# Performance work log

Hardware: AMD Instinct MI355X
Metric: run time of the kernel (lower is better)

## Reference

```python
import jax, jax.numpy as jnp
import numpy as np

B, T, H = 32, 2048, 1024

def setup_inputs() -> dict:
    key = jax.random.key(0)
    ks = jax.random.split(key, 9)
    s = 1.0 / np.sqrt(H)
    return {
        "encoder_outputs": jax.random.normal(ks[0], (B, T, H), jnp.float32),
        "decoder_output": jax.random.normal(ks[1], (1, B, H), jnp.float32),
        "Wk": jax.random.uniform(ks[2], (H, H), jnp.float32, -s, s),
        "bk": jax.random.uniform(ks[3], (H,), jnp.float32, -s, s),
        "Wq": jax.random.uniform(ks[4], (H, H), jnp.float32, -s, s),
        "bq": jax.random.uniform(ks[5], (H,), jnp.float32, -s, s),
        "Wout": jax.random.uniform(ks[6], (H,), jnp.float32, -s, s),
        "bout": jax.random.uniform(ks[7], (), jnp.float32, -s, s),
        "inputs": jax.random.randint(ks[8], (B, T), 0, 32000, jnp.int32),  # unused, as in original
    }

def reference(encoder_outputs, decoder_output, Wk, bk, Wq, bq, Wout, bout, inputs):
    # decoder_output: [1, B, H] -> [B, 1, H]
    dec = jnp.swapaxes(decoder_output, 0, 1)
    k = encoder_outputs @ Wk.T + bk          # [B, T, H]
    q = dec @ Wq.T + bq                      # [B, 1, H]
    score = jnp.tanh(k + q) @ Wout + bout    # [B, T]  (linear_out squeezed)
    attn = jax.nn.softmax(score, axis=-1)    # [B, T]
    context = jnp.einsum('bt,bth->bh', attn, encoder_outputs)  # [B, H]
    return context[:, None, :]               # [B, 1, H]
```

## Files before the change

kernel.cpp:

```cpp
#include <hip/hip_runtime.h>
#include <cmath>
#include <stdint.h>

#define B_ 32
#define T_ 2048
#define H_ 1024

typedef __attribute__((ext_vector_type(8))) __bf16 bf16x8;
typedef __attribute__((ext_vector_type(4))) float f32x4;

__device__ inline void async_copy16(const void* g, void* l) {
    __builtin_amdgcn_global_load_lds((const __attribute__((address_space(1))) uint32_t*)g,
                                     (__attribute__((address_space(3))) uint32_t*)l, 16, 0, 0);
}

__device__ inline float fast_tanh(float x) {
    float e = __expf(2.f * x);
    return 1.f - 2.f / (e + 1.f);
}

__global__ __launch_bounds__(256) void zero_kernel(float* __restrict__ p, int n) {
    int i = blockIdx.x * 256 + threadIdx.x;
    if (i < n) p[i] = 0.f;
}

__global__ __launch_bounds__(256) void convert_kernel(const float* __restrict__ in,
                                                      __bf16* __restrict__ out) {
    size_t i = (size_t)(blockIdx.x * 256 + threadIdx.x) * 8;
    const float4* p = (const float4*)(in + i);
    float4 v0 = p[0], v1 = p[1];
    bf16x8 o;
    o[0] = (__bf16)v0.x; o[1] = (__bf16)v0.y; o[2] = (__bf16)v0.z; o[3] = (__bf16)v0.w;
    o[4] = (__bf16)v1.x; o[5] = (__bf16)v1.y; o[6] = (__bf16)v1.z; o[7] = (__bf16)v1.w;
    *(bf16x8*)(out + i) = o;
}

__global__ __launch_bounds__(256) void q_kernel(const float* __restrict__ dec,
                                                const float* __restrict__ Wq,
                                                const float* __restrict__ bq,
                                                const float* __restrict__ bk,
                                                float* __restrict__ kq) {
    int b = blockIdx.x;
    int hc = blockIdx.y;
    __shared__ float ds[H_];
    for (int i = threadIdx.x; i < H_; i += 256) ds[i] = dec[b * H_ + i];
    __syncthreads();
    int h = hc * 256 + threadIdx.x;
    const float4* w = (const float4*)(Wq + (size_t)h * H_);
    float acc = 0.f;
#pragma unroll 8
    for (int j = 0; j < H_ / 4; j++) {
        float4 v = w[j];
        acc += v.x * ds[4 * j] + v.y * ds[4 * j + 1] + v.z * ds[4 * j + 2] + v.w * ds[4 * j + 3];
    }
    kq[b * H_ + h] = acc + bq[h] + bk[h];
}

__global__ __launch_bounds__(256) void score_mfma(const __bf16* __restrict__ encb,
                                                  const __bf16* __restrict__ Wkb,
                                                  const float* __restrict__ kq,
                                                  const float* __restrict__ Wout,
                                                  float* __restrict__ score) {
    __shared__ __align__(16) __bf16 As[2][512 * 8];
    __shared__ __align__(16) __bf16 Bs[2][512 * 8];

    const int lin = blockIdx.x + 8 * blockIdx.y;
    const int xcd = lin & 7;
    const int j = lin >> 3;
    const int mblk = xcd * 64 + (j >> 3);
    const int hblk = j & 7;
    const int h0 = hblk * 128;
    const int m0 = mblk * 128;
    const int b = m0 >> 11;
    const int tid = threadIdx.x;
    const int lane = tid & 63;
    const int w = tid >> 6;
    const int wm = w & 1, wn = w >> 1;
    const int q4 = lane >> 4, l15 = lane & 15;

    const int S0 = w * 128 + lane;
    const int S1 = S0 + 64;
    const int kg0 = S0 >> 7, row0 = S0 & 127;
    const int kg1 = S1 >> 7, row1 = S1 & 127;
    const __bf16* gA0 = encb + (size_t)(m0 + row0) * H_ + kg0 * 8;
    const __bf16* gA1 = encb + (size_t)(m0 + row1) * H_ + kg1 * 8;
    const __bf16* gB0 = Wkb + (size_t)(h0 + row0) * H_ + kg0 * 8;
    const __bf16* gB1 = Wkb + (size_t)(h0 + row1) * H_ + kg1 * 8;
    const int sA0 = (w * 128) * 8;
    const int sA1 = (w * 128 + 64) * 8;

    f32x4 acc[4][4];
#pragma unroll
    for (int i = 0; i < 4; i++)
#pragma unroll
        for (int jj = 0; jj < 4; jj++) acc[i][jj] = (f32x4){0.f, 0.f, 0.f, 0.f};

#define STAGE(c, kk)                          \
    do {                                      \
        async_copy16(gA0 + (kk), &As[c][sA0]); \
        async_copy16(gA1 + (kk), &As[c][sA1]); \
        async_copy16(gB0 + (kk), &Bs[c][sA0]); \
        async_copy16(gB1 + (kk), &Bs[c][sA1]); \
    } while (0)

#define COMPUTE(c)                                                                        \
    do {                                                                                  \
        bf16x8 a[4], bb[4];                                                               \
        _Pragma("unroll")                                                                 \
        for (int mf = 0; mf < 4; mf++)                                                    \
            a[mf] = *(const bf16x8*)(&As[c][(size_t)(q4 * 128 + wm * 64 + mf * 16 + l15) * 8]); \
        _Pragma("unroll")                                                                 \
        for (int nf = 0; nf < 4; nf++)                                                    \
            bb[nf] = *(const bf16x8*)(&Bs[c][(size_t)(q4 * 128 + wn * 64 + nf * 16 + l15) * 8]); \
        _Pragma("unroll")                                                                 \
        for (int mf = 0; mf < 4; mf++)                                                    \
            _Pragma("unroll")                                                             \
            for (int nf = 0; nf < 4; nf++)                                                \
                acc[mf][nf] =                                                             \
                    __builtin_amdgcn_mfma_f32_16x16x32_bf16(a[mf], bb[nf], acc[mf][nf], 0, 0, 0); \
    } while (0)

    STAGE(0, 0);
    __syncthreads();

    for (int k0 = 0; k0 < H_; k0 += 64) {
        STAGE(1, k0 + 32);
        COMPUTE(0);
        __syncthreads();
        if (k0 + 64 < H_) STAGE(0, k0 + 64);
        COMPUTE(1);
        __syncthreads();
    }
#undef STAGE
#undef COMPUTE

    float wv[4], kqv[4];
#pragma unroll
    for (int nf = 0; nf < 4; nf++) {
        int h = h0 + wn * 64 + nf * 16 + l15;
        wv[nf] = Wout[h];
        kqv[nf] = kq[b * H_ + h];
    }
#pragma unroll
    for (int mf = 0; mf < 4; mf++) {
#pragma unroll
        for (int r = 0; r < 4; r++) {
            float s = 0.f;
#pragma unroll
            for (int nf = 0; nf < 4; nf++)
                s += wv[nf] * fast_tanh(acc[mf][nf][r] + kqv[nf]);
#pragma unroll
            for (int m = 1; m < 16; m <<= 1) s += __shfl_xor(s, m, 64);
            if (l15 == 0)
                atomicAdd(&score[m0 + wm * 64 + mf * 16 + q4 * 4 + r], s);
        }
    }
}

#define BK 32
#define ASTR 68
#define BSTR 132
__global__ __launch_bounds__(256) void score_fp32(const float* __restrict__ enc,
                                                  const float* __restrict__ Wk,
                                                  const float* __restrict__ kq,
                                                  const float* __restrict__ Wout,
                                                  float* __restrict__ score) {
    __shared__ __align__(16) float As[BK * ASTR];
    __shared__ __align__(16) float Bs[BK * BSTR];
    __shared__ float wout_s[128];
    __shared__ float kq_s[128];
    const int m0 = blockIdx.x * 64;
    const int h0 = blockIdx.y * 128;
    const int b = m0 >> 11;
    const int tid = threadIdx.x;
    const int tx = tid & 15;
    const int ty = tid >> 4;
    if (tid < 128) {
        wout_s[tid] = Wout[h0 + tid];
        kq_s[tid] = kq[b * H_ + h0 + tid];
    }
    float acc[4][8];
#pragma unroll
    for (int i = 0; i < 4; i++)
#pragma unroll
        for (int j = 0; j < 8; j++) acc[i][j] = 0.f;
    for (int k0 = 0; k0 < H_; k0 += BK) {
        __syncthreads();
#pragma unroll
        for (int r = 0; r < 2; r++) {
            int li = tid + r * 256;
            int tok = li >> 3, kg = li & 7;
            float4 v = *(const float4*)(enc + (size_t)(m0 + tok) * H_ + k0 + kg * 4);
            As[(kg * 4 + 0) * ASTR + tok] = v.x;
            As[(kg * 4 + 1) * ASTR + tok] = v.y;
            As[(kg * 4 + 2) * ASTR + tok] = v.z;
            As[(kg * 4 + 3) * ASTR + tok] = v.w;
        }
#pragma unroll
        for (int r = 0; r < 4; r++) {
            int li = tid + r * 256;
            int h = li >> 3, kg = li & 7;
            float4 v = *(const float4*)(Wk + (size_t)(h0 + h) * H_ + k0 + kg * 4);
            Bs[(kg * 4 + 0) * BSTR + h] = v.x;
            Bs[(kg * 4 + 1) * BSTR + h] = v.y;
            Bs[(kg * 4 + 2) * BSTR + h] = v.z;
            Bs[(kg * 4 + 3) * BSTR + h] = v.w;
        }
        __syncthreads();
#pragma unroll
        for (int kk = 0; kk < BK; kk++) {
            float4 a4 = *(const float4*)&As[kk * ASTR + ty * 4];
            float4 b4a = *(const float4*)&Bs[kk * BSTR + tx * 4];
            float4 b4b = *(const float4*)&Bs[kk * BSTR + 64 + tx * 4];
            float av[4] = {a4.x, a4.y, a4.z, a4.w};
            float bv[8] = {b4a.x, b4a.y, b4a.z, b4a.w, b4b.x, b4b.y, b4b.z, b4b.w};
#pragma unroll
            for (int i = 0; i < 4; i++)
#pragma unroll
                for (int j = 0; j < 8; j++) acc[i][j] += av[i] * bv[j];
        }
    }
    float wv[8], kqv[8];
#pragma unroll
    for (int j = 0; j < 8; j++) {
        int hl = (j < 4) ? (tx * 4 + j) : (64 + tx * 4 + (j - 4));
        wv[j] = wout_s[hl];
        kqv[j] = kq_s[hl];
    }
#pragma unroll
    for (int i = 0; i < 4; i++) {
        float s = 0.f;
#pragma unroll
        for (int j = 0; j < 8; j++) s += wv[j] * tanhf(acc[i][j] + kqv[j]);
#pragma unroll
        for (int m = 1; m < 16; m <<= 1) s += __shfl_xor(s, m, 64);
        if (tx == 0) atomicAdd(&score[m0 + ty * 4 + i], s);
    }
}

__global__ __launch_bounds__(256) void softmax_kernel(float* __restrict__ score) {
    int b = blockIdx.x, tid = threadIdx.x;
    float* s = score + b * T_;
    __shared__ float red[8];
    float v[8];
    float mx = -1e30f;
#pragma unroll
    for (int i = 0; i < 8; i++) {
        v[i] = s[tid + i * 256];
        mx = fmaxf(mx, v[i]);
    }
#pragma unroll
    for (int m = 32; m >= 1; m >>= 1) mx = fmaxf(mx, __shfl_xor(mx, m, 64));
    if ((tid & 63) == 0) red[tid >> 6] = mx;
    __syncthreads();
    mx = fmaxf(fmaxf(red[0], red[1]), fmaxf(red[2], red[3]));
    float sum = 0.f;
#pragma unroll
    for (int i = 0; i < 8; i++) {
        v[i] = __expf(v[i] - mx);
        sum += v[i];
    }
#pragma unroll
    for (int m = 32; m >= 1; m >>= 1) sum += __shfl_xor(sum, m, 64);
    if ((tid & 63) == 0) red[4 + (tid >> 6)] = sum;
    __syncthreads();
    sum = red[4] + red[5] + red[6] + red[7];
    float inv = 1.f / sum;
#pragma unroll
    for (int i = 0; i < 8; i++) s[tid + i * 256] = v[i] * inv;
}

__global__ __launch_bounds__(256) void context_kernel(const float* __restrict__ enc,
                                                      const float* __restrict__ attn,
                                                      float* __restrict__ out) {
    int ts = blockIdx.x, b = blockIdx.y;
    const float* e = enc + (size_t)b * T_ * H_ + (size_t)ts * 64 * H_ + threadIdx.x * 4;
    const float* a = attn + b * T_ + ts * 64;
    float4 acc = {0.f, 0.f, 0.f, 0.f};
#pragma unroll 4
    for (int t = 0; t < 64; t++) {
        float av = a[t];
        float4 v = *(const float4*)(e + (size_t)t * H_);
        acc.x += av * v.x; acc.y += av * v.y; acc.z += av * v.z; acc.w += av * v.w;
    }
    float* o = out + b * H_ + threadIdx.x * 4;
    atomicAdd(o + 0, acc.x);
    atomicAdd(o + 1, acc.y);
    atomicAdd(o + 2, acc.z);
    atomicAdd(o + 3, acc.w);
}

extern "C" void kernel_launch(void* const* d_in, const int* in_sizes, int n_in,
                              void* d_out, int out_size, void* d_ws, size_t ws_size,
                              hipStream_t stream) {
    const float* enc = (const float*)d_in[0];
    const float* dec = (const float*)d_in[1];
    const float* Wk = (const float*)d_in[2];
    const float* bk = (const float*)d_in[3];
    const float* Wq = (const float*)d_in[4];
    const float* bq = (const float*)d_in[5];
    const float* Wout = (const float*)d_in[6];
    float* out = (float*)d_out;

    const size_t encb_bytes = (size_t)B_ * T_ * H_ * 2;
    const size_t wkb_bytes = (size_t)H_ * H_ * 2;
    const size_t need = encb_bytes + wkb_bytes + (size_t)B_ * H_ * 4 + (size_t)B_ * T_ * 4;

    if (ws_size >= need) {
        __bf16* encb = (__bf16*)d_ws;
        __bf16* Wkb = (__bf16*)((char*)d_ws + encb_bytes);
        float* kq = (float*)((char*)d_ws + encb_bytes + wkb_bytes);
        float* score = kq + B_ * H_;

        convert_kernel<<<(B_ * T_ * H_) / 2048, 256, 0, stream>>>(enc, encb);
        convert_kernel<<<(H_ * H_) / 2048, 256, 0, stream>>>(Wk, Wkb);
        q_kernel<<<dim3(B_, 4), 256, 0, stream>>>(dec, Wq, bq, bk, kq);
        zero_kernel<<<(B_ * T_ + 255) / 256, 256, 0, stream>>>(score, B_ * T_);
        zero_kernel<<<(B_ * H_ + 255) / 256, 256, 0, stream>>>(out, B_ * H_);
        score_mfma<<<dim3(8, 512), 256, 0, stream>>>(encb, Wkb, kq, Wout, score);
        softmax_kernel<<<B_, 256, 0, stream>>>(score);
        context_kernel<<<dim3(32, B_), 256, 0, stream>>>(enc, score, out);
    } else {
        float* kq = (float*)d_ws;
        float* score = kq + B_ * H_;
        q_kernel<<<dim3(B_, 4), 256, 0, stream>>>(dec, Wq, bq, bk, kq);
        zero_kernel<<<(B_ * T_ + 255) / 256, 256, 0, stream>>>(score, B_ * T_);
        zero_kernel<<<(B_ * H_ + 255) / 256, 256, 0, stream>>>(out, B_ * H_);
        score_fp32<<<dim3(1024, 8), 256, 0, stream>>>(enc, Wk, kq, Wout, score);
        softmax_kernel<<<B_, 256, 0, stream>>>(score);
        context_kernel<<<dim3(32, B_), 256, 0, stream>>>(enc, score, out);
    }
}
```

Before: 771.3 us.

## Enlarge score GEMM tile to 256x256 with triple-buffered async LDS pipeline

Reworks the bf16 MFMA score GEMM to use 512-thread blocks, each computing a 256x256 output tile instead of 128x128, so more reuse comes from every LDS load. The LDS staging moves from double to triple buffering with explicit vmcnt waits and raw barriers, which keeps two k-slices in flight. s_setprio is raised around the MFMA bursts. The aim is to cut global and LDS traffic per FLOP and hide load latency, at the cost of more accumulator registers (32 f32x4 per thread), more LDS, and fewer blocks in the grid.

```diff
diff --git a/kernel.cpp b/kernel.cpp
--- a/kernel.cpp
+++ b/kernel.cpp
@@ -56,83 +56,109 @@
     kq[b * H_ + h] = acc + bq[h] + bk[h];
 }
 
-__global__ __launch_bounds__(256) void score_mfma(const __bf16* __restrict__ encb,
-                                                  const __bf16* __restrict__ Wkb,
-                                                  const float* __restrict__ kq,
-                                                  const float* __restrict__ Wout,
-                                                  float* __restrict__ score) {
-    __shared__ __align__(16) __bf16 As[2][512 * 8];
-    __shared__ __align__(16) __bf16 Bs[2][512 * 8];
-
-    const int lin = blockIdx.x + 8 * blockIdx.y;
+__global__ __launch_bounds__(512, 2) void score_mfma(const __bf16* __restrict__ encb,
+                                                     const __bf16* __restrict__ Wkb,
+                                                     const float* __restrict__ kq,
+                                                     const float* __restrict__ Wout,
+                                                     float* __restrict__ score) {
+    __shared__ __align__(16) __bf16 lds[3][16384];
+
+    const int lin = blockIdx.x + 4 * blockIdx.y;
     const int xcd = lin & 7;
-    const int j = lin >> 3;
-    const int mblk = xcd * 64 + (j >> 3);
-    const int hblk = j & 7;
-    const int h0 = hblk * 128;
-    const int m0 = mblk * 128;
+    const int idx = lin >> 3;
+    const int mblk = xcd * 32 + (idx >> 2);
+    const int nblk = idx & 3;
+    const int m0 = mblk * 256;
+    const int h0 = nblk * 256;
     const int b = m0 >> 11;
+
     const int tid = threadIdx.x;
     const int lane = tid & 63;
     const int w = tid >> 6;
-    const int wm = w & 1, wn = w >> 1;
+    const int wm = w >> 2;
+    const int wn = w & 3;
     const int q4 = lane >> 4, l15 = lane & 15;
 
-    const int S0 = w * 128 + lane;
-    const int S1 = S0 + 64;
-    const int kg0 = S0 >> 7, row0 = S0 & 127;
-    const int kg1 = S1 >> 7, row1 = S1 & 127;
-    const __bf16* gA0 = encb + (size_t)(m0 + row0) * H_ + kg0 * 8;
-    const __bf16* gA1 = encb + (size_t)(m0 + row1) * H_ + kg1 * 8;
-    const __bf16* gB0 = Wkb + (size_t)(h0 + row0) * H_ + kg0 * 8;
-    const __bf16* gB1 = Wkb + (size_t)(h0 + row1) * H_ + kg1 * 8;
-    const int sA0 = (w * 128) * 8;
-    const int sA1 = (w * 128 + 64) * 8;
-
-    f32x4 acc[4][4];
-#pragma unroll
-    for (int i = 0; i < 4; i++)
-#pragma unroll
-        for (int jj = 0; jj < 4; jj++) acc[i][jj] = (f32x4){0.f, 0.f, 0.f, 0.f};
-
-#define STAGE(c, kk)                          \
-    do {                                      \
-        async_copy16(gA0 + (kk), &As[c][sA0]); \
-        async_copy16(gA1 + (kk), &As[c][sA1]); \
-        async_copy16(gB0 + (kk), &Bs[c][sA0]); \
-        async_copy16(gB1 + (kk), &Bs[c][sA1]); \
+    const int rowS = tid & 255;
+    const int kgS = tid >> 8;
+    const __bf16* gA0 = encb + (size_t)(m0 + rowS) * H_ + kgS * 8;
+    const __bf16* gA1 = gA0 + 16;
+    const __bf16* gB0 = Wkb + (size_t)(h0 + rowS) * H_ + kgS * 8;
+    const __bf16* gB1 = gB0 + 16;
+    const int sA0 = (w * 64) * 8;
+    const int sA1 = sA0 + 4096;
+    const int sB0 = sA0 + 8192;
+    const int sB1 = sB0 + 4096;
+
+    f32x4 acc[2][4][4];
+#pragma unroll
+    for (int g = 0; g < 2; g++)
+#pragma unroll
+        for (int i = 0; i < 4; i++)
+#pragma unroll
+            for (int jj = 0; jj < 4; jj++) acc[g][i][jj] = (f32x4){0.f, 0.f, 0.f, 0.f};
+
+#define STAGE(jj)                                      \
+    do {                                               \
+        __bf16* Ld = &lds[(jj) % 3][0];                \
+        const int kk = (jj) * 32;                      \
+        async_copy16(gA0 + kk, Ld + sA0);              \
+        async_copy16(gA1 + kk, Ld + sA1);              \
+        async_copy16(gB0 + kk, Ld + sB0);              \
+        async_copy16(gB1 + kk, Ld + sB1);              \
     } while (0)
 
-#define COMPUTE(c)                                                                        \
-    do {                                                                                  \
-        bf16x8 a[4], bb[4];                                                               \
-        _Pragma("unroll")                                                                 \
-        for (int mf = 0; mf < 4; mf++)                                                    \
-            a[mf] = *(const bf16x8*)(&As[c][(size_t)(q4 * 128 + wm * 64 + mf * 16 + l15) * 8]); \
-        _Pragma("unroll")                                                                 \
-        for (int nf = 0; nf < 4; nf++)                                                    \
-            bb[nf] = *(const bf16x8*)(&Bs[c][(size_t)(q4 * 128 + wn * 64 + nf * 16 + l15) * 8]); \
-        _Pragma("unroll")                                                                 \
-        for (int mf = 0; mf < 4; mf++)                                                    \
-            _Pragma("unroll")                                                             \
-            for (int nf = 0; nf < 4; nf++)                                                \
-                acc[mf][nf] =                                                             \
-                    __builtin_amdgcn_mfma_f32_16x16x32_bf16(a[mf], bb[nf], acc[mf][nf], 0, 0, 0); \
-    } while (0)
-
-    STAGE(0, 0);
-    __syncthreads();
-
-    for (int k0 = 0; k0 < H_; k0 += 64) {
-        STAGE(1, k0 + 32);
-        COMPUTE(0);
-        __syncthreads();
-        if (k0 + 64 < H_) STAGE(0, k0 + 64);
-        COMPUTE(1);
-        __syncthreads();
+    STAGE(0);
+    STAGE(1);
+    asm volatile("s_waitcnt vmcnt(4)" ::: "memory");
+    __builtin_amdgcn_s_barrier();
+    __builtin_amdgcn_sched_barrier(0);
+
+    for (int j = 0; j < 32; ++j) {
+        if (j > 0) {
+            if (j < 31) {
+                asm volatile("s_waitcnt vmcnt(4)" ::: "memory");
+            } else {
+                asm volatile("s_waitcnt vmcnt(0)" ::: "memory");
+            }
+            __builtin_amdgcn_s_barrier();
+            __builtin_amdgcn_sched_barrier(0);
+        }
+        const __bf16* L = &lds[j % 3][0];
+        if (j < 30) STAGE(j + 2);
+
+        bf16x8 bfr[4];
+#pragma unroll
+        for (int nf = 0; nf < 4; nf++)
+            bfr[nf] = *(const bf16x8*)(L + 8192 +
+                                       (size_t)(q4 * 256 + wn * 64 + nf * 16 + l15) * 8);
+        bf16x8 afr[4];
+#pragma unroll
+        for (int mf = 0; mf < 4; mf++)
+            afr[mf] = *(const bf16x8*)(L +
+                                       (size_t)(q4 * 256 + wm * 128 + mf * 16 + l15) * 8);
+        __builtin_amdgcn_s_setprio(1);
+#pragma unroll
+        for (int mf = 0; mf < 4; mf++)
+#pragma unroll
+            for (int nf = 0; nf < 4; nf++)
+                acc[0][mf][nf] =
+                    __builtin_amdgcn_mfma_f32_16x16x32_bf16(afr[mf], bfr[nf], acc[0][mf][nf], 0, 0, 0);
+        __builtin_amdgcn_s_setprio(0);
+#pragma unroll
+        for (int mf = 0; mf < 4; mf++)
+            afr[mf] = *(const bf16x8*)(L +
+                                       (size_t)(q4 * 256 + wm * 128 + 64 + mf * 16 + l15) * 8);
+        __builtin_amdgcn_s_setprio(1);
+#pragma unroll
+        for (int mf = 0; mf < 4; mf++)
+#pragma unroll
+            for (int nf = 0; nf < 4; nf++)
+                acc[1][mf][nf] =
+                    __builtin_amdgcn_mfma_f32_16x16x32_bf16(afr[mf], bfr[nf], acc[1][mf][nf], 0, 0, 0);
+        __builtin_amdgcn_s_setprio(0);
     }
 #undef STAGE
-#undef COMPUTE
 
     float wv[4], kqv[4];
 #pragma unroll
@@ -142,17 +168,20 @@
         kqv[nf] = kq[b * H_ + h];
     }
 #pragma unroll
-    for (int mf = 0; mf < 4; mf++) {
-#pragma unroll
-        for (int r = 0; r < 4; r++) {
-            float s = 0.f;
-#pragma unroll
-            for (int nf = 0; nf < 4; nf++)
-                s += wv[nf] * fast_tanh(acc[mf][nf][r] + kqv[nf]);
-#pragma unroll
-            for (int m = 1; m < 16; m <<= 1) s += __shfl_xor(s, m, 64);
-            if (l15 == 0)
-                atomicAdd(&score[m0 + wm * 64 + mf * 16 + q4 * 4 + r], s);
+    for (int g = 0; g < 2; g++) {
+#pragma unroll
+        for (int mf = 0; mf < 4; mf++) {
+#pragma unroll
+            for (int r = 0; r < 4; r++) {
+                float s = 0.f;
+#pragma unroll
+                for (int nf = 0; nf < 4; nf++)
+                    s += wv[nf] * fast_tanh(acc[g][mf][nf][r] + kqv[nf]);
+#pragma unroll
+                for (int m = 1; m < 16; m <<= 1) s += __shfl_xor(s, m, 64);
+                if (l15 == 0)
+                    atomicAdd(&score[m0 + wm * 128 + g * 64 + mf * 16 + q4 * 4 + r], s);
+            }
         }
     }
 }
@@ -317,7 +346,7 @@
         q_kernel<<<dim3(B_, 4), 256, 0, stream>>>(dec, Wq, bq, bk, kq);
         zero_kernel<<<(B_ * T_ + 255) / 256, 256, 0, stream>>>(score, B_ * T_);
         zero_kernel<<<(B_ * H_ + 255) / 256, 256, 0, stream>>>(out, B_ * H_);
-        score_mfma<<<dim3(8, 512), 256, 0, stream>>>(encb, Wkb, kq, Wout, score);
+        score_mfma<<<dim3(4, 256), 512, 0, stream>>>(encb, Wkb, kq, Wout, score);
         softmax_kernel<<<B_, 256, 0, stream>>>(score);
         context_kernel<<<dim3(32, B_), 256, 0, stream>>>(enc, score, out);
     } else {
```

New measurement: 714.2 us. 7.4% less time.
